# Performance work log

Hardware: AMD Instinct MI355X
Metric: run time of the kernel (lower is better)

Reference implementation:

```python
import jax, jax.numpy as jnp
import numpy as np

N = 100000   # number of website nodes
E = 800000   # edges per edge type
F = 128      # in_feats == out_feats
NEG_SLOPE = 0.2


def setup_inputs() -> dict:
    key = jax.random.key(0)
    ks = jax.random.split(key, 16)
    s = 1.0 / np.sqrt(F)
    return {
        "feat": jax.random.normal(ks[0], (N, F), jnp.float32),
        "src_u": jax.random.randint(ks[1], (E,), 0, N),
        "dst_u": jax.random.randint(ks[2], (E,), 0, N),
        "src_r": jax.random.randint(ks[3], (E,), 0, N),
        "dst_r": jax.random.randint(ks[4], (E,), 0, N),
        # fc_self (no bias)
        "W_self": jax.random.uniform(ks[5], (F, F), jnp.float32, -s, s),
        # attn branch 'user'
        "W_u": jax.random.uniform(ks[6], (F, F), jnp.float32, -s, s),
        "a_l_u": jax.random.uniform(ks[7], (F,), jnp.float32, -s, s),
        "a_r_u": jax.random.uniform(ks[8], (F,), jnp.float32, -s, s),
        # attn branch 'reuse'
        "W_r": jax.random.uniform(ks[9], (F, F), jnp.float32, -s, s),
        "a_l_r": jax.random.uniform(ks[10], (F,), jnp.float32, -s, s),
        "a_r_r": jax.random.uniform(ks[11], (F,), jnp.float32, -s, s),
        # fc_neigh (with bias)
        "W_neigh": jax.random.uniform(ks[12], (F, F), jnp.float32, -s, s),
        "b_neigh": jax.random.uniform(ks[13], (F,), jnp.float32, -s, s),
        # module-level bias parameter
        "bias": jnp.zeros((F,), jnp.float32),
    }


def _attn_aggregate(feat, W, a_l, a_r, src, dst, n_nodes):
    """GAT-style single-head aggregation over one edge type.
    Returns [n_nodes, F] = sum_{e: dst(e)=v} softmax_v(leaky_relu(el[src]+er[dst])) * h[src]."""
    h = feat @ W                                    # [N, F] (feat_src == feat_dst)
    el = h @ a_l                                    # [N]
    er = h @ a_r                                    # [N]
    e = jax.nn.leaky_relu(el[src] + er[dst], NEG_SLOPE)   # [E]
    # edge_softmax: normalize over incoming edges of each dst node
    m = jax.ops.segment_max(e, dst, num_segments=n_nodes)  # [N] (-inf for isolated dst, unused)
    ex = jnp.exp(e - m[dst])                        # [E]
    denom = jax.ops.segment_sum(ex, dst, num_segments=n_nodes)  # [N]
    a = ex / denom[dst]                             # [E]
    msg = h[src] * a[:, None]                       # [E, F]
    return jax.ops.segment_sum(msg, dst, num_segments=n_nodes)  # [N, F]


def reference(feat, src_u, dst_u, src_r, dst_r, W_self, W_u, a_l_u, a_r_u,
              W_r, a_l_r, a_r_r, W_neigh, b_neigh, bias):
    n = feat.shape[0]
    neigh_u = _attn_aggregate(feat, W_u, a_l_u, a_r_u, src_u, dst_u, n)
    neigh_r = _attn_aggregate(feat, W_r, a_l_r, a_r_r, src_r, dst_r, n)
    # multi_update_all cross reducer 'mean' over the two edge types
    neigh = 0.5 * (neigh_u + neigh_r)
    h_neigh = neigh @ W_neigh + b_neigh             # fc_neigh
    rst = feat @ W_self + h_neigh                   # fc_self(h_self) + h_neigh
    return rst + bias
```

## Files before the change

kernel.cpp:

```cpp
#include <hip/hip_runtime.h>

#define F 128
#define NEG_SLOPE 0.2f
#define SHIFT 9
#define BPB 512
#define NBS 512

typedef _Float16 f16_t;
typedef _Float16 f16x8 __attribute__((ext_vector_type(8)));
typedef _Float16 f16x2 __attribute__((ext_vector_type(2)));
typedef float f32x4 __attribute__((ext_vector_type(4)));

__global__ __launch_bounds__(128) void prep_mats(
    const float* __restrict__ Wu, const float* __restrict__ Wr,
    const float* __restrict__ Ws, const float* __restrict__ Wn,
    const float* __restrict__ alu, const float* __restrict__ aru,
    const float* __restrict__ alr, const float* __restrict__ arr_,
    f16_t* __restrict__ Mtu, f16_t* __restrict__ Mtr, f16_t* __restrict__ Wts,
    float* __restrict__ wlu, float* __restrict__ wru,
    float* __restrict__ wlr, float* __restrict__ wrr)
{
    int b = blockIdx.x;
    int tid = threadIdx.x;
    if (b < 256) {
        int k = b & 127;
        const float* W = (b < 128) ? Wu : Wr;
        f16_t* M = (b < 128) ? Mtu : Mtr;
        float acc = 0.f;
        for (int t = 0; t < F; t++) acc += W[k * F + t] * Wn[t * F + tid];
        M[tid * F + k] = (f16_t)acc;
    } else if (b < 384) {
        int c = b - 256;
        Wts[c * F + tid] = (f16_t)Ws[tid * F + c];
    } else {
        int which = b - 384;
        const float* W = (which < 2) ? Wu : Wr;
        const float* a = (which == 0) ? alu : (which == 1) ? aru : (which == 2) ? alr : arr_;
        float acc = 0.f;
        for (int c = 0; c < F; c++) acc += W[tid * F + c] * a[c];
        float* o = (which == 0) ? wlu : (which == 1) ? wru : (which == 2) ? wlr : wrr;
        o[tid] = acc;
    }
}


__global__ __launch_bounds__(256) void cast_p1a(
    const float* __restrict__ feat,
    const float* __restrict__ wlu, const float* __restrict__ wru,
    const float* __restrict__ wlr, const float* __restrict__ wrr,
    f16_t* __restrict__ featb,
    float* __restrict__ elu, float* __restrict__ eru,
    float* __restrict__ elr, float* __restrict__ err_,
    const int* __restrict__ dst_u, const int* __restrict__ dst_r,
    int* __restrict__ cnt_bb,
    int Eu, int Et, int N, int chunk, int n, int nbk)
{
    int b = blockIdx.x;
    int tid = threadIdx.x;
    if (b < 256) {
        __shared__ int hist[NBS];
        for (int i = tid; i < NBS; i += 256) hist[i] = 0;
        __syncthreads();
        int e0 = b * chunk;
        int e1 = e0 + chunk; if (e1 > Et) e1 = Et;
        int u1 = (e1 < Eu) ? e1 : Eu;
        for (int e = e0 + tid; e < u1; e += 256) {
            int bin = dst_u[e];
            atomicAdd(&hist[bin >> SHIFT], 1);
        }
        int r0 = (e0 > Eu) ? e0 : Eu;
        for (int e = r0 + tid; e < e1; e += 256) {
            int bin = N + dst_r[e - Eu];
            atomicAdd(&hist[bin >> SHIFT], 1);
        }
        __syncthreads();
        for (int i = tid; i < NBS; i += 256) cnt_bb[b * NBS + i] = hist[i];
        return;
    }
    int fid = b - 256;
    int lane = tid & 63;
    int wave = tid >> 6;
    int lo = lane & 15, hi = lane >> 4;
    int base = fid * 64 + wave * 16;
    if (base >= n) return;
    int row = base + lo;
    if (row > n - 1) row = n - 1;
    const float* fp = feat + (size_t)row * F + hi * 8;
    f16_t* fb = featb + (size_t)row * F + hi * 8;
    const float* wsel = (lo == 0) ? wlu : (lo == 1) ? wru : (lo == 2) ? wlr : wrr;

    f32x4 acc = (f32x4){0.f, 0.f, 0.f, 0.f};
#pragma unroll
    for (int ks = 0; ks < 4; ks++) {
        float4 a0 = *(const float4*)(fp + ks * 32);
        float4 a1 = *(const float4*)(fp + ks * 32 + 4);
        f16x8 af;
        af[0] = (f16_t)a0.x; af[1] = (f16_t)a0.y; af[2] = (f16_t)a0.z; af[3] = (f16_t)a0.w;
        af[4] = (f16_t)a1.x; af[5] = (f16_t)a1.y; af[6] = (f16_t)a1.z; af[7] = (f16_t)a1.w;
        *(f16x8*)(fb + ks * 32) = af;
        f16x8 bf;
#pragma unroll
        for (int q = 0; q < 8; q++) bf[q] = (f16_t)0;
        if (lo < 4) {
            float4 b0 = *(const float4*)(wsel + ks * 32 + hi * 8);
            float4 b1 = *(const float4*)(wsel + ks * 32 + hi * 8 + 4);
            bf[0] = (f16_t)b0.x; bf[1] = (f16_t)b0.y; bf[2] = (f16_t)b0.z; bf[3] = (f16_t)b0.w;
            bf[4] = (f16_t)b1.x; bf[5] = (f16_t)b1.y; bf[6] = (f16_t)b1.z; bf[7] = (f16_t)b1.w;
        }
        acc = __builtin_amdgcn_mfma_f32_16x16x32_f16(af, bf, acc, 0, 0, 0);
    }
    if (lo < 4) {
        float* oarr = (lo == 0) ? elu : (lo == 1) ? eru : (lo == 2) ? elr : err_;
#pragma unroll
        for (int j = 0; j < 4; j++) {
            int r = base + hi * 4 + j;
            if (r < n) oarr[r] = acc[j];
        }
    }
}


__global__ __launch_bounds__(256) void scan_bb1(int* __restrict__ cnt_bb,
                                                int* __restrict__ btot, int nbk)
{
    int k = blockIdx.x;
    int tid = threadIdx.x;
    __shared__ int lds[256];
    int v = cnt_bb[tid * NBS + k];
    lds[tid] = v;
    __syncthreads();
    for (int off = 1; off < 256; off <<= 1) {
        int add = (tid >= off) ? lds[tid - off] : 0;
        __syncthreads();
        lds[tid] += add;
        __syncthreads();
    }
    cnt_bb[tid * NBS + k] = lds[tid] - v;
    if (tid == 255) btot[k] = lds[255];
}

__global__ __launch_bounds__(512) void scan_bb2(const int* __restrict__ btot,
                                                int* __restrict__ bbase,
                                                int* __restrict__ rp,
                                                int nbk, int twoN, int Et)
{
    __shared__ int lds[512];
    int t = threadIdx.x;
    int v = (t < nbk) ? btot[t] : 0;
    lds[t] = v;
    __syncthreads();
    for (int off = 1; off < 512; off <<= 1) {
        int add = (t >= off) ? lds[t - off] : 0;
        __syncthreads();
        lds[t] += add;
        __syncthreads();
    }
    bbase[t] = lds[t] - v;
    if (t == 0) rp[twoN] = Et;
}


__global__ __launch_bounds__(256) void p1b_scatter(
    const int* __restrict__ src_u, const int* __restrict__ dst_u,
    const int* __restrict__ src_r, const int* __restrict__ dst_r,
    const int* __restrict__ cnt_bb, const int* __restrict__ bbase,
    unsigned* __restrict__ bucketed,
    int Eu, int Et, int N, int chunk, int nbk)
{
    int b = blockIdx.x;
    int tid = threadIdx.x;
    __shared__ int cur[NBS];
    for (int i = tid; i < nbk; i += 256) cur[i] = bbase[i] + cnt_bb[b * NBS + i];
    __syncthreads();
    int e0 = b * chunk;
    int e1 = e0 + chunk; if (e1 > Et) e1 = Et;
    int u1 = (e1 < Eu) ? e1 : Eu;
    for (int e = e0 + tid; e < u1; e += 256) {
        int bin = dst_u[e];
        int s = src_u[e];
        int pos = atomicAdd(&cur[bin >> SHIFT], 1);
        bucketed[pos] = (unsigned)s | ((unsigned)(bin & (BPB - 1)) << 17);
    }
    int r0 = (e0 > Eu) ? e0 : Eu;
    for (int e = r0 + tid; e < e1; e += 256) {
        int bin = N + dst_r[e - Eu];
        int s = src_r[e - Eu];
        int pos = atomicAdd(&cur[bin >> SHIFT], 1);
        bucketed[pos] = (unsigned)s | ((unsigned)(bin & (BPB - 1)) << 17);
    }
}


__global__ __launch_bounds__(256) void p2_build(
    const unsigned* __restrict__ bucketed, const int* __restrict__ bbase,
    const float* __restrict__ elu, const float* __restrict__ eru,
    const float* __restrict__ elr, const float* __restrict__ err_,
    int* __restrict__ rp, int* __restrict__ csr, f16_t* __restrict__ exh,
    int twoN, int N)
{
    int k = blockIdx.x;
    int tid = threadIdx.x;
    int beg = bbase[k], end = bbase[k + 1];
    __shared__ int hist[BPB];
    __shared__ int psum[256];
    for (int i = tid; i < BPB; i += 256) hist[i] = 0;
    __syncthreads();
    for (int i = beg + tid; i < end; i += 256) {
        unsigned w = bucketed[i];
        atomicAdd(&hist[(w >> 17) & (BPB - 1)], 1);
    }
    __syncthreads();
    int a0 = hist[2 * tid], a1 = hist[2 * tid + 1];
    psum[tid] = a0 + a1;
    __syncthreads();
    for (int off = 1; off < 256; off <<= 1) {
        int add = (tid >= off) ? psum[tid - off] : 0;
        __syncthreads();
        psum[tid] += add;
        __syncthreads();
    }
    int base0 = beg + psum[tid] - (a0 + a1);
    int bin0 = (k << SHIFT) + 2 * tid;
    if (bin0 < twoN)     rp[bin0]     = base0;
    if (bin0 + 1 < twoN) rp[bin0 + 1] = base0 + a0;
    __syncthreads();
    hist[2 * tid]     = base0;
    hist[2 * tid + 1] = base0 + a0;
    __syncthreads();
    for (int i = beg + tid; i < end; i += 256) {
        unsigned w = bucketed[i];
        int src = (int)(w & 0x1FFFF);
        int binlow = (int)((w >> 17) & (BPB - 1));
        int bin = (k << SHIFT) | binlow;
        bool isu = bin < N;
        const float* el = isu ? elu : elr;
        const float* er = isu ? eru : err_;
        int d = isu ? bin : bin - N;
        float e = el[src] + er[d];
        e = fmaxf(e, NEG_SLOPE * e);
        float ex = __expf(e);
        int pos = atomicAdd(&hist[binlow], 1);
        csr[pos] = src;
        exh[pos] = (f16_t)ex;
    }
}


__global__ __launch_bounds__(256) void aggregate_v2(
    const f16_t* __restrict__ featb, const f16_t* __restrict__ exh,
    const int* __restrict__ rp, const int* __restrict__ csr,
    f16_t* __restrict__ aggu, f16_t* __restrict__ aggr, int n)
{
    int wave = (int)(((size_t)blockIdx.x * 256 + threadIdx.x) >> 6);
    int lane = threadIdx.x & 63;
    int g = lane >> 4, lo = lane & 15;
    int dst = wave * 4 + g;
    bool alive = (dst < n);
    int dc = alive ? dst : (n - 1);

    int begu = rp[dc], endu = rp[dc + 1];
    int begr = rp[n + dc], endr = rp[n + dc + 1];
    if (!alive) { endu = begu; endr = begr; }

    union UV { f16x8 v; f16x2 p[4]; };
    f16x2 z = {(f16_t)0, (f16_t)0};
    f16x2 au0 = z, au1 = z, au2 = z, au3 = z;
    f16x2 ar0 = z, ar1 = z, ar2 = z, ar3 = z;
    float du = 0.f, dr = 0.f;

    int iu = begu, ir = begr;

    int a0 = (iu     < endu) ? iu     : 0;
    int a1 = (iu + 1 < endu) ? iu + 1 : 0;
    int b0 = (ir     < endr) ? ir     : 0;
    int b1 = (ir + 1 < endr) ? ir + 1 : 0;
    int cu0 = csr[a0], cu1 = csr[a1], cr0 = csr[b0], cr1 = csr[b1];
    f16_t wu0 = (iu     < endu) ? exh[a0] : (f16_t)0;
    f16_t wu1 = (iu + 1 < endu) ? exh[a1] : (f16_t)0;
    f16_t wr0 = (ir     < endr) ? exh[b0] : (f16_t)0;
    f16_t wr1 = (ir + 1 < endr) ? exh[b1] : (f16_t)0;
    UV hu0, hu1, hr0, hr1;
    hu0.v = *(const f16x8*)&featb[(size_t)cu0 * F + lo * 8];
    hu1.v = *(const f16x8*)&featb[(size_t)cu1 * F + lo * 8];
    hr0.v = *(const f16x8*)&featb[(size_t)cr0 * F + lo * 8];
    hr1.v = *(const f16x8*)&featb[(size_t)cr1 * F + lo * 8];

    while (iu < endu || ir < endr) {
        int ju = iu + 2, jr = ir + 2;
        int na0 = (ju     < endu) ? ju     : 0;
        int na1 = (ju + 1 < endu) ? ju + 1 : 0;
        int nb0 = (jr     < endr) ? jr     : 0;
        int nb1 = (jr + 1 < endr) ? jr + 1 : 0;
        int ncu0 = csr[na0], ncu1 = csr[na1], ncr0 = csr[nb0], ncr1 = csr[nb1];
        f16_t nwu0 = (ju     < endu) ? exh[na0] : (f16_t)0;
        f16_t nwu1 = (ju + 1 < endu) ? exh[na1] : (f16_t)0;
        f16_t nwr0 = (jr     < endr) ? exh[nb0] : (f16_t)0;
        f16_t nwr1 = (jr + 1 < endr) ? exh[nb1] : (f16_t)0;
        UV pu0, pu1, pr0, pr1;
        pu0.v = *(const f16x8*)&featb[(size_t)ncu0 * F + lo * 8];
        pu1.v = *(const f16x8*)&featb[(size_t)ncu1 * F + lo * 8];
        pr0.v = *(const f16x8*)&featb[(size_t)ncr0 * F + lo * 8];
        pr1.v = *(const f16x8*)&featb[(size_t)ncr1 * F + lo * 8];

        {
            f16x2 wv = {wu0, wu0};
            au0 += wv * hu0.p[0]; au1 += wv * hu0.p[1];
            au2 += wv * hu0.p[2]; au3 += wv * hu0.p[3];
            du += (float)wu0;
        }
        {
            f16x2 wv = {wu1, wu1};
            au0 += wv * hu1.p[0]; au1 += wv * hu1.p[1];
            au2 += wv * hu1.p[2]; au3 += wv * hu1.p[3];
            du += (float)wu1;
        }
        {
            f16x2 wv = {wr0, wr0};
            ar0 += wv * hr0.p[0]; ar1 += wv * hr0.p[1];
            ar2 += wv * hr0.p[2]; ar3 += wv * hr0.p[3];
            dr += (float)wr0;
        }
        {
            f16x2 wv = {wr1, wr1};
            ar0 += wv * hr1.p[0]; ar1 += wv * hr1.p[1];
            ar2 += wv * hr1.p[2]; ar3 += wv * hr1.p[3];
            dr += (float)wr1;
        }

        hu0 = pu0; hu1 = pu1; hr0 = pr0; hr1 = pr1;
        wu0 = nwu0; wu1 = nwu1; wr0 = nwr0; wr1 = nwr1;
        iu = ju; ir = jr;
    }

    if (alive) {
        float invu = (du > 0.f) ? 0.5f / du : 0.f;
        float invr = (dr > 0.f) ? 0.5f / dr : 0.f;
        f16_t ihu = (f16_t)invu, ihr = (f16_t)invr;
        f16x2 ivu = {ihu, ihu}, ivr = {ihr, ihr};
        UV ou, orr;
        ou.p[0] = au0 * ivu; ou.p[1] = au1 * ivu; ou.p[2] = au2 * ivu; ou.p[3] = au3 * ivu;
        orr.p[0] = ar0 * ivr; orr.p[1] = ar1 * ivr; orr.p[2] = ar2 * ivr; orr.p[3] = ar3 * ivr;
        *(f16x8*)&aggu[(size_t)dst * F + lo * 8] = ou.v;
        *(f16x8*)&aggr[(size_t)dst * F + lo * 8] = orr.v;
    }
}


__global__ __launch_bounds__(1024) void mfma_final3(
    const f16_t* __restrict__ featb,
    const f16_t* __restrict__ aggu, const f16_t* __restrict__ aggr,
    const f16_t* __restrict__ Wts, const f16_t* __restrict__ Mtu,
    const f16_t* __restrict__ Mtr,
    const float* __restrict__ bn, const float* __restrict__ bias,
    float* __restrict__ out, int n, int ntiles)
{
    __shared__ f16_t Ls[F * F];
    __shared__ f16_t Lu[F * F];
    __shared__ f16_t Lr[F * F];
    for (int i = threadIdx.x; i < 2048; i += 1024) {
        int c = i >> 4, kc = i & 15, kcs = kc ^ (c & 15);
        *(f16x8*)&Ls[c * F + kcs * 8] = *(const f16x8*)&Wts[c * F + kc * 8];
        *(f16x8*)&Lu[c * F + kcs * 8] = *(const f16x8*)&Mtu[c * F + kc * 8];
        *(f16x8*)&Lr[c * F + kcs * 8] = *(const f16x8*)&Mtr[c * F + kc * 8];
    }
    __syncthreads();

    int lane = threadIdx.x & 63;
    int wave = threadIdx.x >> 6;
    int lo = lane & 15, hi = lane >> 4;

    float cb[8];
#pragma unroll
    for (int t = 0; t < 8; t++) cb[t] = bn[t * 16 + lo] + bias[t * 16 + lo];

    for (int tile = blockIdx.x; tile < ntiles; tile += 256) {
        int row0 = tile * 256 + wave * 16;
        if (row0 >= n) continue;
        int arow = row0 + lo;
        if (arow > n - 1) arow = n - 1;
        const f16_t* pf = featb + (size_t)arow * F + hi * 8;
        const f16_t* pu = aggu + (size_t)arow * F + hi * 8;
        const f16_t* pr = aggr + (size_t)arow * F + hi * 8;

        f32x4 acc[8];
#pragma unroll
        for (int t = 0; t < 8; t++) acc[t] = (f32x4){0.f, 0.f, 0.f, 0.f};

#pragma unroll
        for (int ks = 0; ks < 4; ks++) {
            f16x8 a1 = *(const f16x8*)(pf + ks * 32);
            f16x8 a2 = *(const f16x8*)(pu + ks * 32);
            f16x8 a3 = *(const f16x8*)(pr + ks * 32);
#pragma unroll
            for (int t = 0; t < 8; t++) {
                int c = t * 16 + lo;
                int kcs = (ks * 4 + hi) ^ lo;
                f16x8 bs = *(const f16x8*)&Ls[c * F + kcs * 8];
                f16x8 bu = *(const f16x8*)&Lu[c * F + kcs * 8];
                f16x8 br = *(const f16x8*)&Lr[c * F + kcs * 8];
                acc[t] = __builtin_amdgcn_mfma_f32_16x16x32_f16(a1, bs, acc[t], 0, 0, 0);
                acc[t] = __builtin_amdgcn_mfma_f32_16x16x32_f16(a2, bu, acc[t], 0, 0, 0);
                acc[t] = __builtin_amdgcn_mfma_f32_16x16x32_f16(a3, br, acc[t], 0, 0, 0);
            }
        }

#pragma unroll
        for (int j = 0; j < 4; j++) {
            int r = row0 + hi * 4 + j;
            if (r < n) {
                float* op = out + (size_t)r * F + lo;
#pragma unroll
                for (int t = 0; t < 8; t++) op[t * 16] = acc[t][j] + cb[t];
            }
        }
    }
}


extern "C" void kernel_launch(void* const* d_in, const int* in_sizes, int n_in,
                              void* d_out, int out_size, void* d_ws, size_t ws_size,
                              hipStream_t stream) {
    const float* feat   = (const float*)d_in[0];
    const int*   src_u  = (const int*)d_in[1];
    const int*   dst_u  = (const int*)d_in[2];
    const int*   src_r  = (const int*)d_in[3];
    const int*   dst_r  = (const int*)d_in[4];
    const float* W_self = (const float*)d_in[5];
    const float* W_u    = (const float*)d_in[6];
    const float* a_l_u  = (const float*)d_in[7];
    const float* a_r_u  = (const float*)d_in[8];
    const float* W_r    = (const float*)d_in[9];
    const float* a_l_r  = (const float*)d_in[10];
    const float* a_r_r  = (const float*)d_in[11];
    const float* W_ngh  = (const float*)d_in[12];
    const float* b_ngh  = (const float*)d_in[13];
    const float* bias   = (const float*)d_in[14];
    float* out = (float*)d_out;

    const int N  = in_sizes[0] / F;
    const int Eu = in_sizes[1];
    const int Er = in_sizes[3];
    const int Et = Eu + Er;
    const int twoN = 2 * N;
    const int nbk = (twoN + BPB - 1) >> SHIFT;

    char* ws = (char*)d_ws;
    size_t off = 0;
    auto alloc = [&](size_t bytes) -> void* {
        void* p = ws + off;
        off = (off + bytes + 255) & ~(size_t)255;
        return p;
    };
    f16_t* featb = (f16_t*)alloc((size_t)N * F * 2);
    f16_t* aggu  = (f16_t*)alloc((size_t)N * F * 2);
    f16_t* aggr  = (f16_t*)alloc((size_t)N * F * 2);
    f16_t* Mt_u  = (f16_t*)alloc((size_t)F * F * 2);
    f16_t* Mt_r  = (f16_t*)alloc((size_t)F * F * 2);
    f16_t* Wt_s  = (f16_t*)alloc((size_t)F * F * 2);
    float* wlu = (float*)alloc((size_t)F * 4);
    float* wru = (float*)alloc((size_t)F * 4);
    float* wlr = (float*)alloc((size_t)F * 4);
    float* wrr = (float*)alloc((size_t)F * 4);
    float* elu = (float*)alloc((size_t)N * 4);
    float* eru = (float*)alloc((size_t)N * 4);
    float* elr = (float*)alloc((size_t)N * 4);
    float* err_ = (float*)alloc((size_t)N * 4);
    int* cnt_bb = (int*)alloc((size_t)256 * NBS * 4);
    int* btot   = (int*)alloc((size_t)NBS * 4);
    int* bbase  = (int*)alloc((size_t)(NBS + 1) * 4);
    int* rp2    = (int*)alloc(((size_t)twoN + 1) * 4);
    unsigned* bucketed = (unsigned*)alloc((size_t)Et * 4);
    int* csr2   = (int*)alloc((size_t)Et * 4);
    f16_t* exh  = (f16_t*)alloc((size_t)Et * 2);

    prep_mats<<<388, 128, 0, stream>>>(W_u, W_r, W_self, W_ngh,
                                       a_l_u, a_r_u, a_l_r, a_r_r,
                                       Mt_u, Mt_r, Wt_s, wlu, wru, wlr, wrr);

    const int chunk = (Et + 255) / 256;
    int castBlocks = (N + 63) / 64;
    cast_p1a<<<256 + castBlocks, 256, 0, stream>>>(
        feat, wlu, wru, wlr, wrr, featb, elu, eru, elr, err_,
        dst_u, dst_r, cnt_bb, Eu, Et, N, chunk, N, nbk);

    scan_bb1<<<nbk, 256, 0, stream>>>(cnt_bb, btot, nbk);
    scan_bb2<<<1, 512, 0, stream>>>(btot, bbase, rp2, nbk, twoN, Et);
    p1b_scatter<<<256, 256, 0, stream>>>(src_u, dst_u, src_r, dst_r,
                                         cnt_bb, bbase, bucketed,
                                         Eu, Et, N, chunk, nbk);
    p2_build<<<nbk, 256, 0, stream>>>(bucketed, bbase, elu, eru, elr, err_,
                                      rp2, csr2, exh, twoN, N);

    aggregate_v2<<<(N + 15) / 16, 256, 0, stream>>>(featb, exh, rp2, csr2,
                                                    aggu, aggr, N);
    int ntiles = (N + 255) / 256;
    mfma_final3<<<256, 1024, 0, stream>>>(featb, aggu, aggr,
                                          Wt_s, Mt_u, Mt_r,
                                          b_ngh, bias, out, N, ntiles);
}
```

Before: 158.4 us.

## Move edge-score computation to scatter, widen p2_build, deepen aggregate prefetch

The edge attention exponent is now computed in p1b_scatter, where the edge's src and dst are already at hand, and written to a new bucketed fp16 weight array. p2_build then only permutes the precomputed weights. This removes its branchy el/er gathers and exp, and it runs with 512 threads, one per bin. The aggregate kernel gains a second level of software prefetch: csr indices and weights are loaded two iterations ahead and feature rows one iteration ahead, to hide gather latency. The cost is an extra Et-sized fp16 buffer written and read back, and more registers in the aggregate loop.

```diff
diff --git a/kernel.cpp b/kernel.cpp
--- a/kernel.cpp
+++ b/kernel.cpp
@@ -163,8 +163,10 @@
 __global__ __launch_bounds__(256) void p1b_scatter(
     const int* __restrict__ src_u, const int* __restrict__ dst_u,
     const int* __restrict__ src_r, const int* __restrict__ dst_r,
+    const float* __restrict__ elu, const float* __restrict__ eru,
+    const float* __restrict__ elr, const float* __restrict__ err_,
     const int* __restrict__ cnt_bb, const int* __restrict__ bbase,
-    unsigned* __restrict__ bucketed,
+    unsigned* __restrict__ bucketed, f16_t* __restrict__ wbuck,
     int Eu, int Et, int N, int chunk, int nbk)
 {
     int b = blockIdx.x;
@@ -176,77 +178,73 @@
     int e1 = e0 + chunk; if (e1 > Et) e1 = Et;
     int u1 = (e1 < Eu) ? e1 : Eu;
     for (int e = e0 + tid; e < u1; e += 256) {
-        int bin = dst_u[e];
+        int d = dst_u[e];
         int s = src_u[e];
+        float ev = elu[s] + eru[d];
+        ev = fmaxf(ev, NEG_SLOPE * ev);
+        f16_t w = (f16_t)__expf(ev);
+        int pos = atomicAdd(&cur[d >> SHIFT], 1);
+        bucketed[pos] = (unsigned)s | ((unsigned)(d & (BPB - 1)) << 17);
+        wbuck[pos] = w;
+    }
+    int r0 = (e0 > Eu) ? e0 : Eu;
+    for (int e = r0 + tid; e < e1; e += 256) {
+        int d = dst_r[e - Eu];
+        int s = src_r[e - Eu];
+        int bin = N + d;
+        float ev = elr[s] + err_[d];
+        ev = fmaxf(ev, NEG_SLOPE * ev);
+        f16_t w = (f16_t)__expf(ev);
         int pos = atomicAdd(&cur[bin >> SHIFT], 1);
         bucketed[pos] = (unsigned)s | ((unsigned)(bin & (BPB - 1)) << 17);
-    }
-    int r0 = (e0 > Eu) ? e0 : Eu;
-    for (int e = r0 + tid; e < e1; e += 256) {
-        int bin = N + dst_r[e - Eu];
-        int s = src_r[e - Eu];
-        int pos = atomicAdd(&cur[bin >> SHIFT], 1);
-        bucketed[pos] = (unsigned)s | ((unsigned)(bin & (BPB - 1)) << 17);
-    }
-}
-
-
-__global__ __launch_bounds__(256) void p2_build(
-    const unsigned* __restrict__ bucketed, const int* __restrict__ bbase,
-    const float* __restrict__ elu, const float* __restrict__ eru,
-    const float* __restrict__ elr, const float* __restrict__ err_,
+        wbuck[pos] = w;
+    }
+}
+
+
+__global__ __launch_bounds__(512) void p2_build(
+    const unsigned* __restrict__ bucketed, const f16_t* __restrict__ wbuck,
+    const int* __restrict__ bbase,
     int* __restrict__ rp, int* __restrict__ csr, f16_t* __restrict__ exh,
-    int twoN, int N)
+    int twoN)
 {
     int k = blockIdx.x;
     int tid = threadIdx.x;
     int beg = bbase[k], end = bbase[k + 1];
     __shared__ int hist[BPB];
-    __shared__ int psum[256];
-    for (int i = tid; i < BPB; i += 256) hist[i] = 0;
-    __syncthreads();
-    for (int i = beg + tid; i < end; i += 256) {
+    __shared__ int psum[512];
+    hist[tid] = 0;
+    __syncthreads();
+    for (int i = beg + tid; i < end; i += 512) {
         unsigned w = bucketed[i];
         atomicAdd(&hist[(w >> 17) & (BPB - 1)], 1);
     }
     __syncthreads();
-    int a0 = hist[2 * tid], a1 = hist[2 * tid + 1];
-    psum[tid] = a0 + a1;
-    __syncthreads();
-    for (int off = 1; off < 256; off <<= 1) {
+    int v = hist[tid];
+    psum[tid] = v;
+    __syncthreads();
+    for (int off = 1; off < 512; off <<= 1) {
         int add = (tid >= off) ? psum[tid - off] : 0;
         __syncthreads();
         psum[tid] += add;
         __syncthreads();
     }
-    int base0 = beg + psum[tid] - (a0 + a1);
-    int bin0 = (k << SHIFT) + 2 * tid;
-    if (bin0 < twoN)     rp[bin0]     = base0;
-    if (bin0 + 1 < twoN) rp[bin0 + 1] = base0 + a0;
-    __syncthreads();
-    hist[2 * tid]     = base0;
-    hist[2 * tid + 1] = base0 + a0;
-    __syncthreads();
-    for (int i = beg + tid; i < end; i += 256) {
+    int base = beg + psum[tid] - v;
+    int bin = (k << SHIFT) + tid;
+    if (bin < twoN) rp[bin] = base;
+    hist[tid] = base;
+    __syncthreads();
+    for (int i = beg + tid; i < end; i += 512) {
         unsigned w = bucketed[i];
         int src = (int)(w & 0x1FFFF);
-        int binlow = (int)((w >> 17) & (BPB - 1));
-        int bin = (k << SHIFT) | binlow;
-        bool isu = bin < N;
-        const float* el = isu ? elu : elr;
-        const float* er = isu ? eru : err_;
-        int d = isu ? bin : bin - N;
-        float e = el[src] + er[d];
-        e = fmaxf(e, NEG_SLOPE * e);
-        float ex = __expf(e);
-        int pos = atomicAdd(&hist[binlow], 1);
+        int pos = atomicAdd(&hist[(w >> 17) & (BPB - 1)], 1);
         csr[pos] = src;
-        exh[pos] = (f16_t)ex;
-    }
-}
-
-
-__global__ __launch_bounds__(256) void aggregate_v2(
+        exh[pos] = wbuck[i];
+    }
+}
+
+
+__global__ __launch_bounds__(256) void aggregate_v3(
     const f16_t* __restrict__ featb, const f16_t* __restrict__ exh,
     const int* __restrict__ rp, const int* __restrict__ csr,
     f16_t* __restrict__ aggu, f16_t* __restrict__ aggr, int n)
@@ -270,66 +268,73 @@
 
     int iu = begu, ir = begr;
 
-    int a0 = (iu     < endu) ? iu     : 0;
-    int a1 = (iu + 1 < endu) ? iu + 1 : 0;
-    int b0 = (ir     < endr) ? ir     : 0;
-    int b1 = (ir + 1 < endr) ? ir + 1 : 0;
-    int cu0 = csr[a0], cu1 = csr[a1], cr0 = csr[b0], cr1 = csr[b1];
-    f16_t wu0 = (iu     < endu) ? exh[a0] : (f16_t)0;
-    f16_t wu1 = (iu + 1 < endu) ? exh[a1] : (f16_t)0;
-    f16_t wr0 = (ir     < endr) ? exh[b0] : (f16_t)0;
-    f16_t wr1 = (ir + 1 < endr) ? exh[b1] : (f16_t)0;
+    int aA0 = (iu     < endu) ? iu     : 0, aA1 = (iu + 1 < endu) ? iu + 1 : 0;
+    int bA0 = (ir     < endr) ? ir     : 0, bA1 = (ir + 1 < endr) ? ir + 1 : 0;
+    int cuA0 = csr[aA0], cuA1 = csr[aA1], crA0 = csr[bA0], crA1 = csr[bA1];
+    f16_t wuA0 = (iu     < endu) ? exh[aA0] : (f16_t)0;
+    f16_t wuA1 = (iu + 1 < endu) ? exh[aA1] : (f16_t)0;
+    f16_t wrA0 = (ir     < endr) ? exh[bA0] : (f16_t)0;
+    f16_t wrA1 = (ir + 1 < endr) ? exh[bA1] : (f16_t)0;
+
+    int aB0 = (iu + 2 < endu) ? iu + 2 : 0, aB1 = (iu + 3 < endu) ? iu + 3 : 0;
+    int bB0 = (ir + 2 < endr) ? ir + 2 : 0, bB1 = (ir + 3 < endr) ? ir + 3 : 0;
+    int cuB0 = csr[aB0], cuB1 = csr[aB1], crB0 = csr[bB0], crB1 = csr[bB1];
+    f16_t wuB0 = (iu + 2 < endu) ? exh[aB0] : (f16_t)0;
+    f16_t wuB1 = (iu + 3 < endu) ? exh[aB1] : (f16_t)0;
+    f16_t wrB0 = (ir + 2 < endr) ? exh[bB0] : (f16_t)0;
+    f16_t wrB1 = (ir + 3 < endr) ? exh[bB1] : (f16_t)0;
+
     UV hu0, hu1, hr0, hr1;
-    hu0.v = *(const f16x8*)&featb[(size_t)cu0 * F + lo * 8];
-    hu1.v = *(const f16x8*)&featb[(size_t)cu1 * F + lo * 8];
-    hr0.v = *(const f16x8*)&featb[(size_t)cr0 * F + lo * 8];
-    hr1.v = *(const f16x8*)&featb[(size_t)cr1 * F + lo * 8];
+    hu0.v = *(const f16x8*)&featb[(size_t)cuA0 * F + lo * 8];
+    hu1.v = *(const f16x8*)&featb[(size_t)cuA1 * F + lo * 8];
+    hr0.v = *(const f16x8*)&featb[(size_t)crA0 * F + lo * 8];
+    hr1.v = *(const f16x8*)&featb[(size_t)crA1 * F + lo * 8];
 
     while (iu < endu || ir < endr) {
-        int ju = iu + 2, jr = ir + 2;
-        int na0 = (ju     < endu) ? ju     : 0;
-        int na1 = (ju + 1 < endu) ? ju + 1 : 0;
-        int nb0 = (jr     < endr) ? jr     : 0;
-        int nb1 = (jr + 1 < endr) ? jr + 1 : 0;
-        int ncu0 = csr[na0], ncu1 = csr[na1], ncr0 = csr[nb0], ncr1 = csr[nb1];
-        f16_t nwu0 = (ju     < endu) ? exh[na0] : (f16_t)0;
-        f16_t nwu1 = (ju + 1 < endu) ? exh[na1] : (f16_t)0;
-        f16_t nwr0 = (jr     < endr) ? exh[nb0] : (f16_t)0;
-        f16_t nwr1 = (jr + 1 < endr) ? exh[nb1] : (f16_t)0;
+        int aC0 = (iu + 4 < endu) ? iu + 4 : 0, aC1 = (iu + 5 < endu) ? iu + 5 : 0;
+        int bC0 = (ir + 4 < endr) ? ir + 4 : 0, bC1 = (ir + 5 < endr) ? ir + 5 : 0;
+        int cuC0 = csr[aC0], cuC1 = csr[aC1], crC0 = csr[bC0], crC1 = csr[bC1];
+        f16_t wuC0 = (iu + 4 < endu) ? exh[aC0] : (f16_t)0;
+        f16_t wuC1 = (iu + 5 < endu) ? exh[aC1] : (f16_t)0;
+        f16_t wrC0 = (ir + 4 < endr) ? exh[bC0] : (f16_t)0;
+        f16_t wrC1 = (ir + 5 < endr) ? exh[bC1] : (f16_t)0;
+
         UV pu0, pu1, pr0, pr1;
-        pu0.v = *(const f16x8*)&featb[(size_t)ncu0 * F + lo * 8];
-        pu1.v = *(const f16x8*)&featb[(size_t)ncu1 * F + lo * 8];
-        pr0.v = *(const f16x8*)&featb[(size_t)ncr0 * F + lo * 8];
-        pr1.v = *(const f16x8*)&featb[(size_t)ncr1 * F + lo * 8];
+        pu0.v = *(const f16x8*)&featb[(size_t)cuB0 * F + lo * 8];
+        pu1.v = *(const f16x8*)&featb[(size_t)cuB1 * F + lo * 8];
+        pr0.v = *(const f16x8*)&featb[(size_t)crB0 * F + lo * 8];
+        pr1.v = *(const f16x8*)&featb[(size_t)crB1 * F + lo * 8];
 
         {
-            f16x2 wv = {wu0, wu0};
+            f16x2 wv = {wuA0, wuA0};
             au0 += wv * hu0.p[0]; au1 += wv * hu0.p[1];
             au2 += wv * hu0.p[2]; au3 += wv * hu0.p[3];
-            du += (float)wu0;
+            du += (float)wuA0;
         }
         {
-            f16x2 wv = {wu1, wu1};
+            f16x2 wv = {wuA1, wuA1};
             au0 += wv * hu1.p[0]; au1 += wv * hu1.p[1];
             au2 += wv * hu1.p[2]; au3 += wv * hu1.p[3];
-            du += (float)wu1;
+            du += (float)wuA1;
         }
         {
-            f16x2 wv = {wr0, wr0};
+            f16x2 wv = {wrA0, wrA0};
             ar0 += wv * hr0.p[0]; ar1 += wv * hr0.p[1];
             ar2 += wv * hr0.p[2]; ar3 += wv * hr0.p[3];
-            dr += (float)wr0;
+            dr += (float)wrA0;
         }
         {
-            f16x2 wv = {wr1, wr1};
+            f16x2 wv = {wrA1, wrA1};
             ar0 += wv * hr1.p[0]; ar1 += wv * hr1.p[1];
             ar2 += wv * hr1.p[2]; ar3 += wv * hr1.p[3];
-            dr += (float)wr1;
-        }
-
+            dr += (float)wrA1;
+        }
+
+        wuA0 = wuB0; wuA1 = wuB1; wrA0 = wrB0; wrA1 = wrB1;
+        cuB0 = cuC0; cuB1 = cuC1; crB0 = crC0; crB1 = crC1;
+        wuB0 = wuC0; wuB1 = wuC1; wrB0 = wrC0; wrB1 = wrC1;
         hu0 = pu0; hu1 = pu1; hr0 = pr0; hr1 = pr1;
-        wu0 = nwu0; wu1 = nwu1; wr0 = nwr0; wr1 = nwr1;
-        iu = ju; ir = jr;
+        iu += 2; ir += 2;
     }
 
     if (alive) {
@@ -470,6 +475,7 @@
     int* bbase  = (int*)alloc((size_t)(NBS + 1) * 4);
     int* rp2    = (int*)alloc(((size_t)twoN + 1) * 4);
     unsigned* bucketed = (unsigned*)alloc((size_t)Et * 4);
+    f16_t* wbuck = (f16_t*)alloc((size_t)Et * 2);
     int* csr2   = (int*)alloc((size_t)Et * 4);
     f16_t* exh  = (f16_t*)alloc((size_t)Et * 2);
 
@@ -486,12 +492,13 @@
     scan_bb1<<<nbk, 256, 0, stream>>>(cnt_bb, btot, nbk);
     scan_bb2<<<1, 512, 0, stream>>>(btot, bbase, rp2, nbk, twoN, Et);
     p1b_scatter<<<256, 256, 0, stream>>>(src_u, dst_u, src_r, dst_r,
-                                         cnt_bb, bbase, bucketed,
+                                         elu, eru, elr, err_,
+                                         cnt_bb, bbase, bucketed, wbuck,
                                          Eu, Et, N, chunk, nbk);
-    p2_build<<<nbk, 256, 0, stream>>>(bucketed, bbase, elu, eru, elr, err_,
-                                      rp2, csr2, exh, twoN, N);
-
-    aggregate_v2<<<(N + 15) / 16, 256, 0, stream>>>(featb, exh, rp2, csr2,
+    p2_build<<<nbk, 512, 0, stream>>>(bucketed, wbuck, bbase,
+                                      rp2, csr2, exh, twoN);
+
+    aggregate_v3<<<(N + 15) / 16, 256, 0, stream>>>(featb, exh, rp2, csr2,
                                                     aggu, aggr, N);
     int ntiles = (N + 255) / 256;
     mfma_final3<<<256, 1024, 0, stream>>>(featb, aggu, aggr,
```

Result: slower. 171.0 us (+7.9%).

## Compute edge attention weights inside aggregation instead of storing them in CSR build

Applied to the files above, without the earlier changes.

The CSR build kernel no longer gathers el/er and computes exp per edge, and the fp16 edge-weight array is dropped. Weights are now recomputed in the aggregation kernel from a gather of el[src] plus a per-destination er. The CSR build is also widened to 512 threads, one bin per thread, which simplifies its scan. This removes the 1.6M-element exh write and read, but adds a dependent scalar gather of el[src] inside the aggregation loop, and that gather is not prefetched a step ahead.

```diff
diff --git a/kernel.cpp b/kernel.cpp
--- a/kernel.cpp
+++ b/kernel.cpp
@@ -191,63 +191,49 @@
 }
 
 
-__global__ __launch_bounds__(256) void p2_build(
+__global__ __launch_bounds__(512) void p2_build(
     const unsigned* __restrict__ bucketed, const int* __restrict__ bbase,
-    const float* __restrict__ elu, const float* __restrict__ eru,
-    const float* __restrict__ elr, const float* __restrict__ err_,
-    int* __restrict__ rp, int* __restrict__ csr, f16_t* __restrict__ exh,
-    int twoN, int N)
+    int* __restrict__ rp, int* __restrict__ csr, int twoN)
 {
     int k = blockIdx.x;
     int tid = threadIdx.x;
     int beg = bbase[k], end = bbase[k + 1];
     __shared__ int hist[BPB];
-    __shared__ int psum[256];
-    for (int i = tid; i < BPB; i += 256) hist[i] = 0;
-    __syncthreads();
-    for (int i = beg + tid; i < end; i += 256) {
+    __shared__ int psum[512];
+    hist[tid] = 0;
+    __syncthreads();
+    for (int i = beg + tid; i < end; i += 512) {
         unsigned w = bucketed[i];
         atomicAdd(&hist[(w >> 17) & (BPB - 1)], 1);
     }
     __syncthreads();
-    int a0 = hist[2 * tid], a1 = hist[2 * tid + 1];
-    psum[tid] = a0 + a1;
-    __syncthreads();
-    for (int off = 1; off < 256; off <<= 1) {
+    int v = hist[tid];
+    psum[tid] = v;
+    __syncthreads();
+    for (int off = 1; off < 512; off <<= 1) {
         int add = (tid >= off) ? psum[tid - off] : 0;
         __syncthreads();
         psum[tid] += add;
         __syncthreads();
     }
-    int base0 = beg + psum[tid] - (a0 + a1);
-    int bin0 = (k << SHIFT) + 2 * tid;
-    if (bin0 < twoN)     rp[bin0]     = base0;
-    if (bin0 + 1 < twoN) rp[bin0 + 1] = base0 + a0;
-    __syncthreads();
-    hist[2 * tid]     = base0;
-    hist[2 * tid + 1] = base0 + a0;
-    __syncthreads();
-    for (int i = beg + tid; i < end; i += 256) {
+    int base = beg + psum[tid] - v;
+    int bin = (k << SHIFT) + tid;
+    if (bin < twoN) rp[bin] = base;
+    hist[tid] = base;
+    __syncthreads();
+    for (int i = beg + tid; i < end; i += 512) {
         unsigned w = bucketed[i];
         int src = (int)(w & 0x1FFFF);
-        int binlow = (int)((w >> 17) & (BPB - 1));
-        int bin = (k << SHIFT) | binlow;
-        bool isu = bin < N;
-        const float* el = isu ? elu : elr;
-        const float* er = isu ? eru : err_;
-        int d = isu ? bin : bin - N;
-        float e = el[src] + er[d];
-        e = fmaxf(e, NEG_SLOPE * e);
-        float ex = __expf(e);
-        int pos = atomicAdd(&hist[binlow], 1);
+        int pos = atomicAdd(&hist[(w >> 17) & (BPB - 1)], 1);
         csr[pos] = src;
-        exh[pos] = (f16_t)ex;
-    }
-}
-
-
-__global__ __launch_bounds__(256) void aggregate_v2(
-    const f16_t* __restrict__ featb, const f16_t* __restrict__ exh,
+    }
+}
+
+
+__global__ __launch_bounds__(256) void aggregate_v4(
+    const f16_t* __restrict__ featb,
+    const float* __restrict__ elu, const float* __restrict__ eru,
+    const float* __restrict__ elr, const float* __restrict__ err_,
     const int* __restrict__ rp, const int* __restrict__ csr,
     f16_t* __restrict__ aggu, f16_t* __restrict__ aggr, int n)
 {
@@ -258,9 +244,11 @@
     bool alive = (dst < n);
     int dc = alive ? dst : (n - 1);
 
-    int begu = rp[dc], endu = rp[dc + 1];
-    int begr = rp[n + dc], endr = rp[n + dc + 1];
-    if (!alive) { endu = begu; endr = begr; }
+    int iu = rp[dc], endu = rp[dc + 1];
+    int ir = rp[n + dc], endr = rp[n + dc + 1];
+    if (!alive) { endu = iu; endr = ir; }
+    float ervu = eru[dc];
+    float ervr = err_[dc];
 
     union UV { f16x8 v; f16x2 p[4]; };
     f16x2 z = {(f16_t)0, (f16_t)0};
@@ -268,17 +256,12 @@
     f16x2 ar0 = z, ar1 = z, ar2 = z, ar3 = z;
     float du = 0.f, dr = 0.f;
 
-    int iu = begu, ir = begr;
-
-    int a0 = (iu     < endu) ? iu     : 0;
-    int a1 = (iu + 1 < endu) ? iu + 1 : 0;
-    int b0 = (ir     < endr) ? ir     : 0;
-    int b1 = (ir + 1 < endr) ? ir + 1 : 0;
-    int cu0 = csr[a0], cu1 = csr[a1], cr0 = csr[b0], cr1 = csr[b1];
-    f16_t wu0 = (iu     < endu) ? exh[a0] : (f16_t)0;
-    f16_t wu1 = (iu + 1 < endu) ? exh[a1] : (f16_t)0;
-    f16_t wr0 = (ir     < endr) ? exh[b0] : (f16_t)0;
-    f16_t wr1 = (ir + 1 < endr) ? exh[b1] : (f16_t)0;
+    bool vu0 = iu     < endu, vu1 = iu + 1 < endu;
+    bool vr0 = ir     < endr, vr1 = ir + 1 < endr;
+    int cu0 = csr[vu0 ? iu     : 0];
+    int cu1 = csr[vu1 ? iu + 1 : 0];
+    int cr0 = csr[vr0 ? ir     : 0];
+    int cr1 = csr[vr1 ? ir + 1 : 0];
     UV hu0, hu1, hr0, hr1;
     hu0.v = *(const f16x8*)&featb[(size_t)cu0 * F + lo * 8];
     hu1.v = *(const f16x8*)&featb[(size_t)cu1 * F + lo * 8];
@@ -287,15 +270,12 @@
 
     while (iu < endu || ir < endr) {
         int ju = iu + 2, jr = ir + 2;
-        int na0 = (ju     < endu) ? ju     : 0;
-        int na1 = (ju + 1 < endu) ? ju + 1 : 0;
-        int nb0 = (jr     < endr) ? jr     : 0;
-        int nb1 = (jr + 1 < endr) ? jr + 1 : 0;
-        int ncu0 = csr[na0], ncu1 = csr[na1], ncr0 = csr[nb0], ncr1 = csr[nb1];
-        f16_t nwu0 = (ju     < endu) ? exh[na0] : (f16_t)0;
-        f16_t nwu1 = (ju + 1 < endu) ? exh[na1] : (f16_t)0;
-        f16_t nwr0 = (jr     < endr) ? exh[nb0] : (f16_t)0;
-        f16_t nwr1 = (jr + 1 < endr) ? exh[nb1] : (f16_t)0;
+        bool nvu0 = ju     < endu, nvu1 = ju + 1 < endu;
+        bool nvr0 = jr     < endr, nvr1 = jr + 1 < endr;
+        int ncu0 = csr[nvu0 ? ju     : 0];
+        int ncu1 = csr[nvu1 ? ju + 1 : 0];
+        int ncr0 = csr[nvr0 ? jr     : 0];
+        int ncr1 = csr[nvr1 ? jr + 1 : 0];
         UV pu0, pu1, pr0, pr1;
         pu0.v = *(const f16x8*)&featb[(size_t)ncu0 * F + lo * 8];
         pu1.v = *(const f16x8*)&featb[(size_t)ncu1 * F + lo * 8];
@@ -303,32 +283,41 @@
         pr1.v = *(const f16x8*)&featb[(size_t)ncr1 * F + lo * 8];
 
         {
-            f16x2 wv = {wu0, wu0};
+            float e = elu[cu0] + ervu; e = fmaxf(e, NEG_SLOPE * e);
+            float ex = vu0 ? __expf(e) : 0.f;
+            f16_t w = (f16_t)ex; f16x2 wv = {w, w};
             au0 += wv * hu0.p[0]; au1 += wv * hu0.p[1];
             au2 += wv * hu0.p[2]; au3 += wv * hu0.p[3];
-            du += (float)wu0;
+            du += ex;
         }
         {
-            f16x2 wv = {wu1, wu1};
+            float e = elu[cu1] + ervu; e = fmaxf(e, NEG_SLOPE * e);
+            float ex = vu1 ? __expf(e) : 0.f;
+            f16_t w = (f16_t)ex; f16x2 wv = {w, w};
             au0 += wv * hu1.p[0]; au1 += wv * hu1.p[1];
             au2 += wv * hu1.p[2]; au3 += wv * hu1.p[3];
-            du += (float)wu1;
+            du += ex;
         }
         {
-            f16x2 wv = {wr0, wr0};
+            float e = elr[cr0] + ervr; e = fmaxf(e, NEG_SLOPE * e);
+            float ex = vr0 ? __expf(e) : 0.f;
+            f16_t w = (f16_t)ex; f16x2 wv = {w, w};
             ar0 += wv * hr0.p[0]; ar1 += wv * hr0.p[1];
             ar2 += wv * hr0.p[2]; ar3 += wv * hr0.p[3];
-            dr += (float)wr0;
+            dr += ex;
         }
         {
-            f16x2 wv = {wr1, wr1};
+            float e = elr[cr1] + ervr; e = fmaxf(e, NEG_SLOPE * e);
+            float ex = vr1 ? __expf(e) : 0.f;
+            f16_t w = (f16_t)ex; f16x2 wv = {w, w};
             ar0 += wv * hr1.p[0]; ar1 += wv * hr1.p[1];
             ar2 += wv * hr1.p[2]; ar3 += wv * hr1.p[3];
-            dr += (float)wr1;
+            dr += ex;
         }
 
         hu0 = pu0; hu1 = pu1; hr0 = pr0; hr1 = pr1;
-        wu0 = nwu0; wu1 = nwu1; wr0 = nwr0; wr1 = nwr1;
+        cu0 = ncu0; cu1 = ncu1; cr0 = ncr0; cr1 = ncr1;
+        vu0 = nvu0; vu1 = nvu1; vr0 = nvr0; vr1 = nvr1;
         iu = ju; ir = jr;
     }
 
@@ -471,7 +460,6 @@
     int* rp2    = (int*)alloc(((size_t)twoN + 1) * 4);
     unsigned* bucketed = (unsigned*)alloc((size_t)Et * 4);
     int* csr2   = (int*)alloc((size_t)Et * 4);
-    f16_t* exh  = (f16_t*)alloc((size_t)Et * 2);
 
     prep_mats<<<388, 128, 0, stream>>>(W_u, W_r, W_self, W_ngh,
                                        a_l_u, a_r_u, a_l_r, a_r_r,
@@ -488,11 +476,10 @@
     p1b_scatter<<<256, 256, 0, stream>>>(src_u, dst_u, src_r, dst_r,
                                          cnt_bb, bbase, bucketed,
                                          Eu, Et, N, chunk, nbk);
-    p2_build<<<nbk, 256, 0, stream>>>(bucketed, bbase, elu, eru, elr, err_,
-                                      rp2, csr2, exh, twoN, N);
-
-    aggregate_v2<<<(N + 15) / 16, 256, 0, stream>>>(featb, exh, rp2, csr2,
-                                                    aggu, aggr, N);
+    p2_build<<<nbk, 512, 0, stream>>>(bucketed, bbase, rp2, csr2, twoN);
+
+    aggregate_v4<<<(N + 15) / 16, 256, 0, stream>>>(featb, elu, eru, elr, err_,
+                                                    rp2, csr2, aggu, aggr, N);
     int ntiles = (N + 255) / 256;
     mfma_final3<<<256, 1024, 0, stream>>>(featb, aggu, aggr,
                                           Wt_s, Mt_u, Mt_r,
```

Measured after the change: 150.7 us. 1.05x faster.
